# Kernel optimization log

Measured on AMD Instinct MI355X. Metric: run time of the kernel, lower is better.

The kernel has to match this reference:

```python
import jax, jax.numpy as jnp
import numpy as np

B = 2048        # patients (segments)
K = 4           # images per patient
C = 1280        # backbone_out (tf_efficientnet_b0)
PAIRS = K * (K - 1) // 2  # torch.combinations -> 6
NCLS = 1
N_DROP = 5


def setup_inputs() -> dict:
    key = jax.random.key(0)
    ks = jax.random.split(key, 8)
    x = jax.random.normal(ks[0], (B * K, C), jnp.float32)  # detached backbone features
    ids2 = jnp.repeat(jnp.arange(B, dtype=jnp.int32), PAIRS)  # segment id per pair
    Wc = jax.random.normal(ks[1], (C, C, 2), jnp.float32) * 0.02  # Conv1d(C,C,k=2) weight
    bc = jnp.zeros((C,), jnp.float32)
    W0 = jax.random.normal(ks[2], (NCLS, C), jnp.float32) * 0.02
    b0 = jnp.zeros((NCLS,), jnp.float32)
    W1 = jax.random.normal(ks[3], (1, C), jnp.float32) * 0.02
    b1 = jnp.zeros((1,), jnp.float32)
    W2 = jax.random.normal(ks[4], (1, C), jnp.float32) * 0.02
    b2 = jnp.zeros((1,), jnp.float32)
    return dict(x=x, ids2=ids2, Wc=Wc, bc=bc, W0=W0, b0=b0, W1=W1, b1=b1, W2=W2, b2=b2)


def reference(x, ids2, Wc, bc, W0, b0, W1, b1, W2, b2):
    # --- pair combinations within each patient group of K images ---
    ii, jj = np.triu_indices(K, 1)               # static [PAIRS]
    xg = x.reshape(B, K, C)
    xa = xg[:, ii].reshape(B * PAIRS, C)         # first element of each pair
    xb = xg[:, jj].reshape(B * PAIRS, C)         # second element
    # Conv1d(C, C, kernel=2) over the length-2 pair sequence + ReLU
    xc = jax.nn.relu(xa @ Wc[:, :, 0].T + xb @ Wc[:, :, 1].T + bc)  # [P, C]

    # --- 5 fixed dropout masks (p=0.5, train-mode scaling) ---
    masks = jax.random.bernoulli(jax.random.key(42), 0.5,
                                 (N_DROP, xc.shape[0], C)).astype(xc.dtype) * 2.0
    xd = xc[None] * masks                        # [D, P, C]

    cnt = jax.ops.segment_sum(jnp.ones_like(ids2, dtype=xc.dtype),
                              ids2, num_segments=B)  # [B], == PAIRS

    def agg(W, b):
        # head -> scalar mean over classes -> segment-mean over pairs -> mean over dropouts
        z = (jnp.einsum('dpc,oc->dpo', xd, W) + b).mean(-1)          # [D, P]
        s = jax.vmap(lambda u: jax.ops.segment_sum(u, ids2, num_segments=B))(z)
        return (s / cnt).mean(0)                                      # [B]

    logits = agg(W0, b0)
    logits1 = agg(W1, b1)
    logits2 = agg(W2, b2)
    return jnp.stack([logits, logits1, logits2], axis=1)  # [B, 3]
```

## Files before the change

### kernel.cpp

```cpp
#include <hip/hip_runtime.h>


typedef __attribute__((ext_vector_type(8))) short short8;
typedef __attribute__((ext_vector_type(4))) float f32x4;

#define PLANE 15728640u
#define KS2   (0x1BD11BDAu ^ 42u)

__device__ __forceinline__ unsigned short f2bf(float f) {
  unsigned int u = __builtin_bit_cast(unsigned int, f);
  u = (u + 0x7FFFu + ((u >> 16) & 1u)) >> 16;
  return (unsigned short)u;
}
__device__ __forceinline__ float bf2f(unsigned short h) {
  unsigned int u = ((unsigned int)h) << 16;
  return __builtin_bit_cast(float, u);
}

__global__ __launch_bounds__(256) void prep(
    const float* __restrict__ x, unsigned short* __restrict__ xb,
    const float* __restrict__ Wc, unsigned short* __restrict__ Wb) {
  const int bid = blockIdx.x;
  const int t = threadIdx.x;
  if (bid < 2560) {
#pragma unroll
    for (int p = 0; p < 4; p++) {
      const int i4 = bid * 1024 + p * 256 + t;
      const float4 v = ((const float4*)x)[i4];
      ushort4 o;
      o.x = f2bf(v.x); o.y = f2bf(v.y); o.z = f2bf(v.z); o.w = f2bf(v.w);
      ((ushort4*)xb)[i4] = o;
    }
  } else {
    const int i = (bid - 2560) * 256 + t;
    const int n = i / 640;
    const int cin = (i - n * 640) * 2;
    const float4 v = *(const float4*)(Wc + n * 2560 + cin * 2);
    *(ushort2*)(Wb + n * 2560 + cin) =
        make_ushort2(f2bf(v.x), f2bf(v.z));
    *(ushort2*)(Wb + n * 2560 + 1280 + cin) =
        make_ushort2(f2bf(v.y), f2bf(v.w));
  }
}

__device__ __forceinline__ unsigned int rotl(unsigned int x, int r) {
  return __builtin_amdgcn_alignbit(x, x, 32 - r);
}

__device__ __forceinline__ unsigned int tf_msb6(const unsigned int cbase) {
  unsigned int x0[6], x1[6];
#pragma unroll
  for (int q = 0; q < 6; q++) {
    const unsigned int c = cbase + (unsigned int)q * 2048u;
    x0[q] = c;
    x1[q] = rotl(c, 13) ^ c;
  }
#define R6(r)                                                   \
  _Pragma("unroll") for (int q = 0; q < 6; q++) {               \
    x0[q] += x1[q];                                             \
    x1[q] = rotl(x1[q], (r)) ^ x0[q];                           \
  }
  R6(15) R6(26) R6(6)
#pragma unroll
  for (int q = 0; q < 6; q++) {
    const unsigned int u = x1[q] + (KS2 + 1u);
    x0[q] = x0[q] + u + 42u;
    x1[q] = rotl(u, 17) ^ x0[q];
  }
  R6(29) R6(16) R6(24)
#pragma unroll
  for (int q = 0; q < 6; q++) {
    const unsigned int u = x1[q] + 2u;
    x0[q] = x0[q] + u + KS2;
    x1[q] = rotl(u, 13) ^ x0[q];
  }
  R6(15) R6(26) R6(6)
#pragma unroll
  for (int q = 0; q < 6; q++) {
    const unsigned int u = x1[q] + 45u;
    x0[q] = x0[q] + u;
    x1[q] = rotl(u, 17) ^ x0[q];
  }
  R6(29) R6(16) R6(24)
#pragma unroll
  for (int q = 0; q < 6; q++) {
    const unsigned int u = x1[q] + (KS2 + 4u);
    x0[q] = x0[q] + u + 42u;
    x1[q] = rotl(u, 13) ^ x0[q];
  }
  R6(15) R6(26) R6(6)
#undef R6
  unsigned int bits = 0;
#pragma unroll
  for (int q = 0; q < 6; q++)
    bits |= (((x0[q] + KS2) ^ (x1[q] + 5u)) >> 31) << q;
  return bits;
}

#define GL_LDS(g, l) __builtin_amdgcn_global_load_lds( \
    (const __attribute__((address_space(1))) unsigned int*)(g), \
    (__attribute__((address_space(3))) unsigned int*)(l), 16, 0, 0)

__global__ __launch_bounds__(256) void mixed(
    const unsigned short* __restrict__ Xb,
    const unsigned short* __restrict__ Wb,
    unsigned short* __restrict__ U0b,
    unsigned short* __restrict__ U1b,
    unsigned int* __restrict__ Spk)
{
  __shared__ unsigned short sA[128 * 32];
  __shared__ unsigned short sB[128 * 32];
  const int bid = blockIdx.x;
  const int t = threadIdx.x;

  const int id = bid;
  const int xcd = id & 7;
  const int slot = id >> 3;
  const int mband = xcd * 8 + slot / 20;
  const int nst = slot % 20;
  const int side = nst / 10;
  const int n0 = (nst % 10) * 128;
  const int p0 = mband * 128;

  const int lane = t & 63, w = t >> 6;
  const int wr = w >> 1, wc = w & 1;
  const int mrow = lane & 15;
  const int koff = (lane >> 4) * 8;
  const int srow = lane >> 2, schk = (lane & 3) * 8;

  unsigned short* const ldsA0 = sA + (w * 32 + 0) * 32;
  unsigned short* const ldsA1 = sA + (w * 32 + 16) * 32;
  unsigned short* const ldsB0 = sB + (w * 32 + 0) * 32;
  unsigned short* const ldsB1 = sB + (w * 32 + 16) * 32;
  const unsigned short* const gA0 = Xb + (p0 + w * 32 + srow) * 1280 + schk;
  const unsigned short* const gA1 = Xb + (p0 + w * 32 + 16 + srow) * 1280 + schk;
  const unsigned short* const gB0 =
      Wb + (n0 + w * 32 + srow) * 2560 + side * 1280 + schk;
  const unsigned short* const gB1 =
      Wb + (n0 + w * 32 + 16 + srow) * 2560 + side * 1280 + schk;

  f32x4 acc[4][4];
#pragma unroll
  for (int i = 0; i < 4; i++)
#pragma unroll
    for (int j = 0; j < 4; j++) acc[i][j] = (f32x4){0.f, 0.f, 0.f, 0.f};

  unsigned int zacc[6] = {0u, 0u, 0u, 0u, 0u, 0u};
  const unsigned int c8 = ((unsigned int)bid * 1536u + (unsigned int)t) * 8u;

  for (int k0 = 0; k0 < 1280; k0 += 32) {
    __syncthreads();
    GL_LDS(gA0 + k0, ldsA0);
    GL_LDS(gA1 + k0, ldsA1);
    GL_LDS(gB0 + k0, ldsB0);
    GL_LDS(gB1 + k0, ldsB1);
    {
      const int ks = k0 >> 5;
      const int sub = ks & 7;
      const int dpl = ks >> 3;
      const unsigned int bits =
          tf_msb6(c8 + (unsigned int)sub + 42u + (unsigned int)dpl * PLANE);
#pragma unroll
      for (int q = 0; q < 6; q++)
        zacc[q] += ((bits >> q) & 1u) << (4 * sub);
    }
    __syncthreads();
    short8 af[4], bfr[4];
#pragma unroll
    for (int i = 0; i < 4; i++)
      af[i] = *(const short8*)(sA + (wr * 64 + i * 16 + mrow) * 32 + koff);
#pragma unroll
    for (int j = 0; j < 4; j++)
      bfr[j] = *(const short8*)(sB + (wc * 64 + j * 16 + mrow) * 32 + koff);
#pragma unroll
    for (int i = 0; i < 4; i++)
#pragma unroll
      for (int j = 0; j < 4; j++)
        acc[i][j] = __builtin_amdgcn_mfma_f32_16x16x32_bf16(af[i], bfr[j],
                                                            acc[i][j], 0, 0, 0);
  }

#pragma unroll
  for (int q = 0; q < 6; q++)
    Spk[bid * 1536 + q * 256 + t] = zacc[q];

  unsigned short* const U = side ? U1b : U0b;
  const int mq = (lane >> 4) * 4;
  const int nn = lane & 15;
#pragma unroll
  for (int j = 0; j < 4; j++) {
    const int n = n0 + wc * 64 + j * 16 + nn;
#pragma unroll
    for (int i = 0; i < 4; i++) {
      const int prow = p0 + wr * 64 + i * 16 + mq;
#pragma unroll
      for (int rg = 0; rg < 4; rg++)
        U[(prow + rg) * 1280 + n] = f2bf(acc[i][j][rg]);
    }
  }
}

__global__ __launch_bounds__(256) void combine(
    const unsigned short* __restrict__ U0b, const unsigned short* __restrict__ U1b,
    const unsigned int* __restrict__ Spk, const float* __restrict__ bc,
    const float* __restrict__ W0, const float* __restrict__ W1,
    const float* __restrict__ W2,
    const float* __restrict__ b0, const float* __restrict__ b1,
    const float* __restrict__ b2, float* __restrict__ out)
{
  const int pat = blockIdx.x;
  const int t = threadIdx.x;
  const int rbase = pat * 4 * 1280;
  const int sbase = pat * 6 * 160;
  float s0 = 0.f, s1 = 0.f, s2 = 0.f;

  for (int qi = 0; qi < 5; qi++) {
    const int c = qi * 256 + t;
    const float w0 = W0[c], w1 = W1[c], w2 = W2[c], bcv = bc[c];
    const float u00 = bf2f(U0b[rbase + c]);
    const float u01 = bf2f(U0b[rbase + 1280 + c]);
    const float u02 = bf2f(U0b[rbase + 2560 + c]);
    const float u11 = bf2f(U1b[rbase + 1280 + c]);
    const float u12 = bf2f(U1b[rbase + 2560 + c]);
    const float u13 = bf2f(U1b[rbase + 3840 + c]);
    const float pv[6] = {u00 + u11, u00 + u12, u00 + u13,
                         u01 + u12, u01 + u13, u02 + u13};
    const int cd = c >> 3, cn = 4 * (c & 7);
#pragma unroll
    for (int pr = 0; pr < 6; pr++) {
      float v = pv[pr] + bcv;
      v = v > 0.f ? v : 0.f;
      const int z = (int)((Spk[sbase + pr * 160 + cd] >> cn) & 7u);
      const float tx = v * (float)(5 - z);
      s0 += tx * w0; s1 += tx * w1; s2 += tx * w2;
    }
  }

#pragma unroll
  for (int off = 32; off > 0; off >>= 1) {
    s0 += __shfl_xor(s0, off); s1 += __shfl_xor(s1, off); s2 += __shfl_xor(s2, off);
  }
  __shared__ float red[4][3];
  const int lane = t & 63, w = t >> 6;
  if (lane == 0) { red[w][0] = s0; red[w][1] = s1; red[w][2] = s2; }
  __syncthreads();
  if (t == 0) {
    const float r0 = red[0][0] + red[1][0] + red[2][0] + red[3][0];
    const float r1 = red[0][1] + red[1][1] + red[2][1] + red[3][1];
    const float r2 = red[0][2] + red[1][2] + red[2][2] + red[3][2];
    out[pat * 3 + 0] = b0[0] + r0 * (1.0f / 15.0f);
    out[pat * 3 + 1] = b1[0] + r1 * (1.0f / 15.0f);
    out[pat * 3 + 2] = b2[0] + r2 * (1.0f / 15.0f);
  }
}

extern "C" void kernel_launch(void* const* d_in, const int* in_sizes, int n_in,
                              void* d_out, int out_size, void* d_ws, size_t ws_size,
                              hipStream_t stream) {
  const float* x  = (const float*)d_in[0];
  const float* Wc = (const float*)d_in[2];
  const float* bc = (const float*)d_in[3];
  const float* W0 = (const float*)d_in[4];
  const float* b0 = (const float*)d_in[5];
  const float* W1 = (const float*)d_in[6];
  const float* b1 = (const float*)d_in[7];
  const float* W2 = (const float*)d_in[8];
  const float* b2 = (const float*)d_in[9];
  float* out = (float*)d_out;

  char* ws = (char*)d_ws;
  unsigned short* xb  = (unsigned short*)ws;
  unsigned short* Wb  = (unsigned short*)(ws + 20971520);
  unsigned short* U0b = (unsigned short*)(ws + 27525120);
  unsigned short* U1b = (unsigned short*)(ws + 48496640);
  unsigned int*   Spk = (unsigned int*)(ws + 69468160);

  prep<<<5760, 256, 0, stream>>>(x, xb, Wc, Wb);
  mixed<<<1280, 256, 0, stream>>>(xb, Wb, U0b, U1b, Spk);
  combine<<<2048, 256, 0, stream>>>(U0b, U1b, Spk, bc, W0, W1, W2,
                                    b0, b1, b2, out);
}
```

Before: 279.0 us.

## Fuse prep, GEMM and combine into one cooperative persistent kernel

```diff
diff --git a/kernel.cpp b/kernel.cpp
--- a/kernel.cpp
+++ b/kernel.cpp
@@ -1,4 +1,7 @@
 #include <hip/hip_runtime.h>
+#include <hip/hip_cooperative_groups.h>
+
+namespace cg = cooperative_groups;
 
 
 typedef __attribute__((ext_vector_type(8))) short short8;
@@ -15,6 +18,208 @@
 __device__ __forceinline__ float bf2f(unsigned short h) {
   unsigned int u = ((unsigned int)h) << 16;
   return __builtin_bit_cast(float, u);
+}
+
+__device__ __forceinline__ unsigned int rotl(unsigned int x, int r) {
+  return __builtin_amdgcn_alignbit(x, x, 32 - r);
+}
+
+__device__ __forceinline__ unsigned int tf_msb6(const unsigned int cbase) {
+  unsigned int x0[6], x1[6];
+#pragma unroll
+  for (int q = 0; q < 6; q++) {
+    const unsigned int c = cbase + (unsigned int)q * 2048u;
+    x0[q] = c;
+    x1[q] = rotl(c, 13) ^ c;
+  }
+#define R6(r)                                                   \
+  _Pragma("unroll") for (int q = 0; q < 6; q++) {               \
+    x0[q] += x1[q];                                             \
+    x1[q] = rotl(x1[q], (r)) ^ x0[q];                           \
+  }
+  R6(15) R6(26) R6(6)
+#pragma unroll
+  for (int q = 0; q < 6; q++) {
+    const unsigned int u = x1[q] + (KS2 + 1u);
+    x0[q] = x0[q] + u + 42u;
+    x1[q] = rotl(u, 17) ^ x0[q];
+  }
+  R6(29) R6(16) R6(24)
+#pragma unroll
+  for (int q = 0; q < 6; q++) {
+    const unsigned int u = x1[q] + 2u;
+    x0[q] = x0[q] + u + KS2;
+    x1[q] = rotl(u, 13) ^ x0[q];
+  }
+  R6(15) R6(26) R6(6)
+#pragma unroll
+  for (int q = 0; q < 6; q++) {
+    const unsigned int u = x1[q] + 45u;
+    x0[q] = x0[q] + u;
+    x1[q] = rotl(u, 17) ^ x0[q];
+  }
+  R6(29) R6(16) R6(24)
+#pragma unroll
+  for (int q = 0; q < 6; q++) {
+    const unsigned int u = x1[q] + (KS2 + 4u);
+    x0[q] = x0[q] + u + 42u;
+    x1[q] = rotl(u, 13) ^ x0[q];
+  }
+  R6(15) R6(26) R6(6)
+#undef R6
+  unsigned int bits = 0;
+#pragma unroll
+  for (int q = 0; q < 6; q++)
+    bits |= (((x0[q] + KS2) ^ (x1[q] + 5u)) >> 31) << q;
+  return bits;
+}
+
+#define GL_LDS(g, l) __builtin_amdgcn_global_load_lds( \
+    (const __attribute__((address_space(1))) unsigned int*)(g), \
+    (__attribute__((address_space(3))) unsigned int*)(l), 16, 0, 0)
+
+
+__device__ __forceinline__ void gemm_rng_tile(
+    const int tile, const int t,
+    unsigned short* sA, unsigned short* sB,
+    const unsigned short* Xb, const unsigned short* Wb,
+    unsigned short* U0b, unsigned short* U1b, unsigned int* Spk)
+{
+  const int xcd = tile & 7;
+  const int slot = tile >> 3;
+  const int mband = xcd * 8 + slot / 20;
+  const int nst = slot % 20;
+  const int side = nst / 10;
+  const int n0 = (nst % 10) * 128;
+  const int p0 = mband * 128;
+
+  const int lane = t & 63, w = t >> 6;
+  const int wr = w >> 1, wc = w & 1;
+  const int mrow = lane & 15;
+  const int koff = (lane >> 4) * 8;
+  const int srow = lane >> 2, schk = (lane & 3) * 8;
+
+  unsigned short* const ldsA0 = sA + (w * 32 + 0) * 32;
+  unsigned short* const ldsA1 = sA + (w * 32 + 16) * 32;
+  unsigned short* const ldsB0 = sB + (w * 32 + 0) * 32;
+  unsigned short* const ldsB1 = sB + (w * 32 + 16) * 32;
+  const unsigned short* const gA0 = Xb + (p0 + w * 32 + srow) * 1280 + schk;
+  const unsigned short* const gA1 = Xb + (p0 + w * 32 + 16 + srow) * 1280 + schk;
+  const unsigned short* const gB0 =
+      Wb + (n0 + w * 32 + srow) * 2560 + side * 1280 + schk;
+  const unsigned short* const gB1 =
+      Wb + (n0 + w * 32 + 16 + srow) * 2560 + side * 1280 + schk;
+
+  f32x4 acc[4][4];
+#pragma unroll
+  for (int i = 0; i < 4; i++)
+#pragma unroll
+    for (int j = 0; j < 4; j++) acc[i][j] = (f32x4){0.f, 0.f, 0.f, 0.f};
+
+  unsigned int zacc[6] = {0u, 0u, 0u, 0u, 0u, 0u};
+  const unsigned int c8 = ((unsigned int)tile * 1536u + (unsigned int)t) * 8u;
+
+  for (int k0 = 0; k0 < 1280; k0 += 32) {
+    __syncthreads();
+    GL_LDS(gA0 + k0, ldsA0);
+    GL_LDS(gA1 + k0, ldsA1);
+    GL_LDS(gB0 + k0, ldsB0);
+    GL_LDS(gB1 + k0, ldsB1);
+    {
+      const int ks = k0 >> 5;
+      const int sub = ks & 7;
+      const int dpl = ks >> 3;
+      const unsigned int bits =
+          tf_msb6(c8 + (unsigned int)sub + 42u + (unsigned int)dpl * PLANE);
+#pragma unroll
+      for (int q = 0; q < 6; q++)
+        zacc[q] += ((bits >> q) & 1u) << (4 * sub);
+    }
+    __syncthreads();
+    short8 af[4], bfr[4];
+#pragma unroll
+    for (int i = 0; i < 4; i++)
+      af[i] = *(const short8*)(sA + (wr * 64 + i * 16 + mrow) * 32 + koff);
+#pragma unroll
+    for (int j = 0; j < 4; j++)
+      bfr[j] = *(const short8*)(sB + (wc * 64 + j * 16 + mrow) * 32 + koff);
+#pragma unroll
+    for (int i = 0; i < 4; i++)
+#pragma unroll
+      for (int j = 0; j < 4; j++)
+        acc[i][j] = __builtin_amdgcn_mfma_f32_16x16x32_bf16(af[i], bfr[j],
+                                                            acc[i][j], 0, 0, 0);
+  }
+
+#pragma unroll
+  for (int q = 0; q < 6; q++)
+    Spk[tile * 1536 + q * 256 + t] = zacc[q];
+
+  unsigned short* const U = side ? U1b : U0b;
+  const int mq = (lane >> 4) * 4;
+  const int nn = lane & 15;
+#pragma unroll
+  for (int j = 0; j < 4; j++) {
+    const int n = n0 + wc * 64 + j * 16 + nn;
+#pragma unroll
+    for (int i = 0; i < 4; i++) {
+      const int prow = p0 + wr * 64 + i * 16 + mq;
+#pragma unroll
+      for (int rg = 0; rg < 4; rg++)
+        U[(prow + rg) * 1280 + n] = f2bf(acc[i][j][rg]);
+    }
+  }
+}
+
+__device__ __forceinline__ void combine_pat(
+    const int pat, const int t, float (*red)[3],
+    const unsigned short* U0b, const unsigned short* U1b,
+    const unsigned int* Spk, const float* bc,
+    const float* W0, const float* W1, const float* W2,
+    const float* b0, const float* b1, const float* b2, float* out)
+{
+  const int rbase = pat * 4 * 1280;
+  const int sbase = pat * 6 * 160;
+  float s0 = 0.f, s1 = 0.f, s2 = 0.f;
+
+  for (int qi = 0; qi < 5; qi++) {
+    const int c = qi * 256 + t;
+    const float w0 = W0[c], w1 = W1[c], w2 = W2[c], bcv = bc[c];
+    const float u00 = bf2f(U0b[rbase + c]);
+    const float u01 = bf2f(U0b[rbase + 1280 + c]);
+    const float u02 = bf2f(U0b[rbase + 2560 + c]);
+    const float u11 = bf2f(U1b[rbase + 1280 + c]);
+    const float u12 = bf2f(U1b[rbase + 2560 + c]);
+    const float u13 = bf2f(U1b[rbase + 3840 + c]);
+    const float pv[6] = {u00 + u11, u00 + u12, u00 + u13,
+                         u01 + u12, u01 + u13, u02 + u13};
+    const int cd = c >> 3, cn = 4 * (c & 7);
+#pragma unroll
+    for (int pr = 0; pr < 6; pr++) {
+      float v = pv[pr] + bcv;
+      v = v > 0.f ? v : 0.f;
+      const int z = (int)((Spk[sbase + pr * 160 + cd] >> cn) & 7u);
+      const float tx = v * (float)(5 - z);
+      s0 += tx * w0; s1 += tx * w1; s2 += tx * w2;
+    }
+  }
+
+#pragma unroll
+  for (int off = 32; off > 0; off >>= 1) {
+    s0 += __shfl_xor(s0, off); s1 += __shfl_xor(s1, off); s2 += __shfl_xor(s2, off);
+  }
+  const int lane = t & 63, w = t >> 6;
+  if (lane == 0) { red[w][0] = s0; red[w][1] = s1; red[w][2] = s2; }
+  __syncthreads();
+  if (t == 0) {
+    const float r0 = red[0][0] + red[1][0] + red[2][0] + red[3][0];
+    const float r1 = red[0][1] + red[1][1] + red[2][1] + red[3][1];
+    const float r2 = red[0][2] + red[1][2] + red[2][2] + red[3][2];
+    out[pat * 3 + 0] = b0[0] + r0 * (1.0f / 15.0f);
+    out[pat * 3 + 1] = b1[0] + r1 * (1.0f / 15.0f);
+    out[pat * 3 + 2] = b2[0] + r2 * (1.0f / 15.0f);
+  }
+  __syncthreads();
 }
 
 __global__ __launch_bounds__(256) void prep(
@@ -43,161 +248,14 @@
   }
 }
 
-__device__ __forceinline__ unsigned int rotl(unsigned int x, int r) {
-  return __builtin_amdgcn_alignbit(x, x, 32 - r);
-}
-
-__device__ __forceinline__ unsigned int tf_msb6(const unsigned int cbase) {
-  unsigned int x0[6], x1[6];
-#pragma unroll
-  for (int q = 0; q < 6; q++) {
-    const unsigned int c = cbase + (unsigned int)q * 2048u;
-    x0[q] = c;
-    x1[q] = rotl(c, 13) ^ c;
-  }
-#define R6(r)                                                   \
-  _Pragma("unroll") for (int q = 0; q < 6; q++) {               \
-    x0[q] += x1[q];                                             \
-    x1[q] = rotl(x1[q], (r)) ^ x0[q];                           \
-  }
-  R6(15) R6(26) R6(6)
-#pragma unroll
-  for (int q = 0; q < 6; q++) {
-    const unsigned int u = x1[q] + (KS2 + 1u);
-    x0[q] = x0[q] + u + 42u;
-    x1[q] = rotl(u, 17) ^ x0[q];
-  }
-  R6(29) R6(16) R6(24)
-#pragma unroll
-  for (int q = 0; q < 6; q++) {
-    const unsigned int u = x1[q] + 2u;
-    x0[q] = x0[q] + u + KS2;
-    x1[q] = rotl(u, 13) ^ x0[q];
-  }
-  R6(15) R6(26) R6(6)
-#pragma unroll
-  for (int q = 0; q < 6; q++) {
-    const unsigned int u = x1[q] + 45u;
-    x0[q] = x0[q] + u;
-    x1[q] = rotl(u, 17) ^ x0[q];
-  }
-  R6(29) R6(16) R6(24)
-#pragma unroll
-  for (int q = 0; q < 6; q++) {
-    const unsigned int u = x1[q] + (KS2 + 4u);
-    x0[q] = x0[q] + u + 42u;
-    x1[q] = rotl(u, 13) ^ x0[q];
-  }
-  R6(15) R6(26) R6(6)
-#undef R6
-  unsigned int bits = 0;
-#pragma unroll
-  for (int q = 0; q < 6; q++)
-    bits |= (((x0[q] + KS2) ^ (x1[q] + 5u)) >> 31) << q;
-  return bits;
-}
-
-#define GL_LDS(g, l) __builtin_amdgcn_global_load_lds( \
-    (const __attribute__((address_space(1))) unsigned int*)(g), \
-    (__attribute__((address_space(3))) unsigned int*)(l), 16, 0, 0)
-
 __global__ __launch_bounds__(256) void mixed(
-    const unsigned short* __restrict__ Xb,
-    const unsigned short* __restrict__ Wb,
-    unsigned short* __restrict__ U0b,
-    unsigned short* __restrict__ U1b,
+    const unsigned short* __restrict__ Xb, const unsigned short* __restrict__ Wb,
+    unsigned short* __restrict__ U0b, unsigned short* __restrict__ U1b,
     unsigned int* __restrict__ Spk)
 {
   __shared__ unsigned short sA[128 * 32];
   __shared__ unsigned short sB[128 * 32];
-  const int bid = blockIdx.x;
-  const int t = threadIdx.x;
-
-  const int id = bid;
-  const int xcd = id & 7;
-  const int slot = id >> 3;
-  const int mband = xcd * 8 + slot / 20;
-  const int nst = slot % 20;
-  const int side = nst / 10;
-  const int n0 = (nst % 10) * 128;
-  const int p0 = mband * 128;
-
-  const int lane = t & 63, w = t >> 6;
-  const int wr = w >> 1, wc = w & 1;
-  const int mrow = lane & 15;
-  const int koff = (lane >> 4) * 8;
-  const int srow = lane >> 2, schk = (lane & 3) * 8;
-
-  unsigned short* const ldsA0 = sA + (w * 32 + 0) * 32;
-  unsigned short* const ldsA1 = sA + (w * 32 + 16) * 32;
-  unsigned short* const ldsB0 = sB + (w * 32 + 0) * 32;
-  unsigned short* const ldsB1 = sB + (w * 32 + 16) * 32;
-  const unsigned short* const gA0 = Xb + (p0 + w * 32 + srow) * 1280 + schk;
-  const unsigned short* const gA1 = Xb + (p0 + w * 32 + 16 + srow) * 1280 + schk;
-  const unsigned short* const gB0 =
-      Wb + (n0 + w * 32 + srow) * 2560 + side * 1280 + schk;
-  const unsigned short* const gB1 =
-      Wb + (n0 + w * 32 + 16 + srow) * 2560 + side * 1280 + schk;
-
-  f32x4 acc[4][4];
-#pragma unroll
-  for (int i = 0; i < 4; i++)
-#pragma unroll
-    for (int j = 0; j < 4; j++) acc[i][j] = (f32x4){0.f, 0.f, 0.f, 0.f};
-
-  unsigned int zacc[6] = {0u, 0u, 0u, 0u, 0u, 0u};
-  const unsigned int c8 = ((unsigned int)bid * 1536u + (unsigned int)t) * 8u;
-
-  for (int k0 = 0; k0 < 1280; k0 += 32) {
-    __syncthreads();
-    GL_LDS(gA0 + k0, ldsA0);
-    GL_LDS(gA1 + k0, ldsA1);
-    GL_LDS(gB0 + k0, ldsB0);
-    GL_LDS(gB1 + k0, ldsB1);
-    {
-      const int ks = k0 >> 5;
-      const int sub = ks & 7;
-      const int dpl = ks >> 3;
-      const unsigned int bits =
-          tf_msb6(c8 + (unsigned int)sub + 42u + (unsigned int)dpl * PLANE);
-#pragma unroll
-      for (int q = 0; q < 6; q++)
-        zacc[q] += ((bits >> q) & 1u) << (4 * sub);
-    }
-    __syncthreads();
-    short8 af[4], bfr[4];
-#pragma unroll
-    for (int i = 0; i < 4; i++)
-      af[i] = *(const short8*)(sA + (wr * 64 + i * 16 + mrow) * 32 + koff);
-#pragma unroll
-    for (int j = 0; j < 4; j++)
-      bfr[j] = *(const short8*)(sB + (wc * 64 + j * 16 + mrow) * 32 + koff);
-#pragma unroll
-    for (int i = 0; i < 4; i++)
-#pragma unroll
-      for (int j = 0; j < 4; j++)
-        acc[i][j] = __builtin_amdgcn_mfma_f32_16x16x32_bf16(af[i], bfr[j],
-                                                            acc[i][j], 0, 0, 0);
-  }
-
-#pragma unroll
-  for (int q = 0; q < 6; q++)
-    Spk[bid * 1536 + q * 256 + t] = zacc[q];
-
-  unsigned short* const U = side ? U1b : U0b;
-  const int mq = (lane >> 4) * 4;
-  const int nn = lane & 15;
-#pragma unroll
-  for (int j = 0; j < 4; j++) {
-    const int n = n0 + wc * 64 + j * 16 + nn;
-#pragma unroll
-    for (int i = 0; i < 4; i++) {
-      const int prow = p0 + wr * 64 + i * 16 + mq;
-#pragma unroll
-      for (int rg = 0; rg < 4; rg++)
-        U[(prow + rg) * 1280 + n] = f2bf(acc[i][j][rg]);
-    }
-  }
+  gemm_rng_tile(blockIdx.x, threadIdx.x, sA, sB, Xb, Wb, U0b, U1b, Spk);
 }
 
 __global__ __launch_bounds__(256) void combine(
@@ -208,50 +266,55 @@
     const float* __restrict__ b0, const float* __restrict__ b1,
     const float* __restrict__ b2, float* __restrict__ out)
 {
-  const int pat = blockIdx.x;
+  __shared__ float red[4][3];
+  combine_pat(blockIdx.x, threadIdx.x, red, U0b, U1b, Spk, bc,
+              W0, W1, W2, b0, b1, b2, out);
+}
+
+__global__ __launch_bounds__(256, 5) void fused(
+    const float* __restrict__ x, const float* __restrict__ Wc,
+    unsigned short* __restrict__ xb, unsigned short* __restrict__ Wb,
+    unsigned short* __restrict__ U0b, unsigned short* __restrict__ U1b,
+    unsigned int* __restrict__ Spk,
+    const float* __restrict__ bc,
+    const float* __restrict__ W0, const float* __restrict__ W1,
+    const float* __restrict__ W2,
+    const float* __restrict__ b0, const float* __restrict__ b1,
+    const float* __restrict__ b2, float* __restrict__ out)
+{
+  __shared__ unsigned short sA[128 * 32];
+  __shared__ unsigned short sB[128 * 32];
+  __shared__ float red[4][3];
+  const int bid = blockIdx.x;
   const int t = threadIdx.x;
-  const int rbase = pat * 4 * 1280;
-  const int sbase = pat * 6 * 160;
-  float s0 = 0.f, s1 = 0.f, s2 = 0.f;
-
-  for (int qi = 0; qi < 5; qi++) {
-    const int c = qi * 256 + t;
-    const float w0 = W0[c], w1 = W1[c], w2 = W2[c], bcv = bc[c];
-    const float u00 = bf2f(U0b[rbase + c]);
-    const float u01 = bf2f(U0b[rbase + 1280 + c]);
-    const float u02 = bf2f(U0b[rbase + 2560 + c]);
-    const float u11 = bf2f(U1b[rbase + 1280 + c]);
-    const float u12 = bf2f(U1b[rbase + 2560 + c]);
-    const float u13 = bf2f(U1b[rbase + 3840 + c]);
-    const float pv[6] = {u00 + u11, u00 + u12, u00 + u13,
-                         u01 + u12, u01 + u13, u02 + u13};
-    const int cd = c >> 3, cn = 4 * (c & 7);
-#pragma unroll
-    for (int pr = 0; pr < 6; pr++) {
-      float v = pv[pr] + bcv;
-      v = v > 0.f ? v : 0.f;
-      const int z = (int)((Spk[sbase + pr * 160 + cd] >> cn) & 7u);
-      const float tx = v * (float)(5 - z);
-      s0 += tx * w0; s1 += tx * w1; s2 += tx * w2;
-    }
-  }
-
-#pragma unroll
-  for (int off = 32; off > 0; off >>= 1) {
-    s0 += __shfl_xor(s0, off); s1 += __shfl_xor(s1, off); s2 += __shfl_xor(s2, off);
-  }
-  __shared__ float red[4][3];
-  const int lane = t & 63, w = t >> 6;
-  if (lane == 0) { red[w][0] = s0; red[w][1] = s1; red[w][2] = s2; }
-  __syncthreads();
-  if (t == 0) {
-    const float r0 = red[0][0] + red[1][0] + red[2][0] + red[3][0];
-    const float r1 = red[0][1] + red[1][1] + red[2][1] + red[3][1];
-    const float r2 = red[0][2] + red[1][2] + red[2][2] + red[3][2];
-    out[pat * 3 + 0] = b0[0] + r0 * (1.0f / 15.0f);
-    out[pat * 3 + 1] = b1[0] + r1 * (1.0f / 15.0f);
-    out[pat * 3 + 2] = b2[0] + r2 * (1.0f / 15.0f);
-  }
+  const int stride = gridDim.x * 256;
+  cg::grid_group gr = cg::this_grid();
+
+  for (int i4 = bid * 256 + t; i4 < 2621440; i4 += stride) {
+    const float4 v = ((const float4*)x)[i4];
+    ushort4 o;
+    o.x = f2bf(v.x); o.y = f2bf(v.y); o.z = f2bf(v.z); o.w = f2bf(v.w);
+    ((ushort4*)xb)[i4] = o;
+  }
+  for (int i = bid * 256 + t; i < 819200; i += stride) {
+    const int n = i / 640;
+    const int cin = (i - n * 640) * 2;
+    const float4 v = *(const float4*)(Wc + n * 2560 + cin * 2);
+    *(ushort2*)(Wb + n * 2560 + cin) =
+        make_ushort2(f2bf(v.x), f2bf(v.z));
+    *(ushort2*)(Wb + n * 2560 + 1280 + cin) =
+        make_ushort2(f2bf(v.y), f2bf(v.w));
+  }
+  __threadfence();
+  gr.sync();
+
+  for (int tile = bid; tile < 1280; tile += gridDim.x)
+    gemm_rng_tile(tile, t, sA, sB, xb, Wb, U0b, U1b, Spk);
+  __threadfence();
+  gr.sync();
+
+  for (int pat = bid; pat < 2048; pat += gridDim.x)
+    combine_pat(pat, t, red, U0b, U1b, Spk, bc, W0, W1, W2, b0, b1, b2, out);
 }
 
 extern "C" void kernel_launch(void* const* d_in, const int* in_sizes, int n_in,
@@ -275,8 +338,31 @@
   unsigned short* U1b = (unsigned short*)(ws + 48496640);
   unsigned int*   Spk = (unsigned int*)(ws + 69468160);
 
-  prep<<<5760, 256, 0, stream>>>(x, xb, Wc, Wb);
-  mixed<<<1280, 256, 0, stream>>>(xb, Wb, U0b, U1b, Spk);
-  combine<<<2048, 256, 0, stream>>>(U0b, U1b, Spk, bc, W0, W1, W2,
-                                    b0, b1, b2, out);
-}
+  static int max_blocks_per_cu = -2;
+  if (max_blocks_per_cu == -2) {
+    int mb = 0;
+    hipError_t qe = hipOccupancyMaxActiveBlocksPerMultiprocessor(
+        &mb, (const void*)fused, 256, 0);
+    max_blocks_per_cu = (qe == hipSuccess && mb > 0) ? mb : -1;
+  }
+
+  bool coop_ok = false;
+  if (max_blocks_per_cu > 0) {
+    int NB = max_blocks_per_cu * 256;
+    if (NB > 1280) NB = 1280;
+    void* args[] = {(void*)&x,  (void*)&Wc, (void*)&xb, (void*)&Wb,
+                    (void*)&U0b, (void*)&U1b, (void*)&Spk, (void*)&bc,
+                    (void*)&W0, (void*)&W1, (void*)&W2,
+                    (void*)&b0, (void*)&b1, (void*)&b2, (void*)&out};
+    hipError_t e = hipLaunchCooperativeKernel((const void*)fused, dim3(NB),
+                                              dim3(256), args, 0, stream);
+    coop_ok = (e == hipSuccess);
+  }
+
+  if (!coop_ok) {
+    prep<<<5760, 256, 0, stream>>>(x, xb, Wc, Wb);
+    mixed<<<1280, 256, 0, stream>>>(xb, Wb, U0b, U1b, Spk);
+    combine<<<2048, 256, 0, stream>>>(U0b, U1b, Spk, bc, W0, W1, W2,
+                                      b0, b1, b2, out);
+  }
+}
```

Result: slower. 649.8 us (+132.9%).
